# Kernel optimization log

Measured on AMD Instinct MI355X. Metric: run time of the kernel, lower is better.

The kernel has to match this reference:

```python
import jax, jax.numpy as jnp
import numpy as np

B, C = 16384, 5000
EPS = 1e-6
NEG_BIG = -1e30  # stand-in for -inf so rows with no positives stay finite


def setup_inputs() -> dict:
    key = jax.random.key(0)
    k1, k2, k3 = jax.random.split(key, 3)
    inp = jax.random.normal(k1, (B, C), dtype=jnp.float32)
    target = jax.random.randint(k2, (B, C), 0, 2, dtype=jnp.int32)
    weights = jax.random.uniform(k3, (B,), dtype=jnp.float32)
    return {"input": inp, "target": target, "weights": weights}


def reference(input, target, weights):
    # loss_ij = target_ij * log(clamp(sigmoid(x_ij), eps, 1-eps))
    logp = jnp.log(jnp.clip(jax.nn.sigmoid(input), EPS, 1.0 - EPS))  # [B, C], all < 0
    t = target.astype(logp.dtype)
    pos = t > 0
    # Original code: for rows with k positives, take max of loss over the positive
    # labels, then abs (entries are negative, so abs == negate). For k == 1 the
    # -sum over the row equals the same thing. Rows with zero positives stay 0.
    masked = jnp.where(pos, logp, NEG_BIG)            # [B, C]
    row_max = jnp.max(masked, axis=1)                 # [B]
    has_pos = jnp.any(pos, axis=1)                    # [B]
    loss1 = jnp.where(has_pos, -row_max, 0.0)         # [B], non-negative
    loss1 = loss1 * weights                           # instance-wise weights
    return jnp.mean(loss1)                            # aggregate='mean'
```

## Files before the change

kernel.cpp:

```cpp
#include <hip/hip_runtime.h>


#define NROWS 16384
#define NCOLS 5000
#define NVEC  (NCOLS / 4)
#define EPSF  1e-6f

typedef float fvec4 __attribute__((ext_vector_type(4)));
typedef int   ivec4 __attribute__((ext_vector_type(4)));

__global__ __launch_bounds__(256) void row_loss_kernel(
    const float* __restrict__ inp,
    const int*   __restrict__ tgt,
    const float* __restrict__ w,
    float*       __restrict__ row_loss)
{
    const int lane = threadIdx.x & 63;
    const int wid  = threadIdx.x >> 6;
    const int wave_global = blockIdx.x * 4 + wid;
    const float NEG = -3.0e38f;

    #pragma unroll
    for (int rr = 0; rr < 2; ++rr) {
        const int row = wave_global * 2 + rr;
        const fvec4* __restrict__ x4 = (const fvec4*)(inp + (size_t)row * NCOLS);
        const ivec4* __restrict__ t4 = (const ivec4*)(tgt + (size_t)row * NCOLS);

        float m = NEG;
        #pragma unroll
        for (int g = 0; g < 4; ++g) {
            fvec4 xv[5];
            ivec4 tv[5];
            #pragma unroll
            for (int k = 0; k < 5; ++k) {
                const int idx = (g * 5 + k) * 64 + lane;
                if (idx < NVEC) {
                    xv[k] = __builtin_nontemporal_load(x4 + idx);
                    tv[k] = __builtin_nontemporal_load(t4 + idx);
                } else {
                    xv[k] = (fvec4)0.0f;
                    tv[k] = (ivec4)0;
                }
            }
            #pragma unroll
            for (int k = 0; k < 5; ++k) {
                m = fmaxf(m, (tv[k][0] > 0) ? xv[k][0] : NEG);
                m = fmaxf(m, (tv[k][1] > 0) ? xv[k][1] : NEG);
                m = fmaxf(m, (tv[k][2] > 0) ? xv[k][2] : NEG);
                m = fmaxf(m, (tv[k][3] > 0) ? xv[k][3] : NEG);
            }
        }

        #pragma unroll
        for (int off = 32; off > 0; off >>= 1)
            m = fmaxf(m, __shfl_xor(m, off, 64));

        if (lane == 0) {
            float loss = 0.0f;
            if (m > -1.0e38f) {
                float p = 1.0f / (1.0f + __expf(-m));
                p = fminf(fmaxf(p, EPSF), 1.0f - EPSF);
                loss = -logf(p) * w[row];
            }
            row_loss[row] = loss;
        }
    }
}

__global__ __launch_bounds__(1024) void reduce_mean_kernel(
    const float* __restrict__ row_loss,
    float*       __restrict__ out)
{
    const fvec4* __restrict__ rl4 = (const fvec4*)row_loss;
    float s = 0.0f;
    #pragma unroll
    for (int j = 0; j < 4; ++j) {
        fvec4 v = rl4[threadIdx.x + j * 1024];
        s += (v[0] + v[1]) + (v[2] + v[3]);
    }

    #pragma unroll
    for (int off = 32; off > 0; off >>= 1)
        s += __shfl_xor(s, off, 64);

    __shared__ float ssum[16];
    const int lane = threadIdx.x & 63;
    const int wid  = threadIdx.x >> 6;
    if (lane == 0) ssum[wid] = s;
    __syncthreads();

    if (threadIdx.x == 0) {
        float tot = 0.0f;
        #pragma unroll
        for (int i = 0; i < 16; ++i) tot += ssum[i];
        out[0] = tot / (float)NROWS;
    }
}

extern "C" void kernel_launch(void* const* d_in, const int* in_sizes, int n_in,
                              void* d_out, int out_size, void* d_ws, size_t ws_size,
                              hipStream_t stream) {
    const float* inp = (const float*)d_in[0];
    const int*   tgt = (const int*)d_in[1];
    const float* w   = (const float*)d_in[2];
    float* row_loss  = (float*)d_ws;
    float* out       = (float*)d_out;

    row_loss_kernel<<<2048, 256, 0, stream>>>(inp, tgt, w, row_loss);
    reduce_mean_kernel<<<1, 1024, 0, stream>>>(row_loss, out);
}
```

Baseline: 565.7 us.

## Software-pipeline row loads with double buffers and one row per wave

Each wave now handles a single row, and the grid doubles to 4096 blocks. Loads are double-buffered so the next group of five vectors is in flight while the previous group is reduced. Four independent max accumulators shorten the dependency chain, and the per-load bounds checks are replaced by one tail-specific load. The aim is more memory-level parallelism and better latency hiding in a bandwidth-bound pass, at the cost of higher register pressure, which the launch-bounds occupancy hint tries to contain.

```diff
diff --git a/kernel.cpp b/kernel.cpp
--- a/kernel.cpp
+++ b/kernel.cpp
@@ -5,11 +5,58 @@
 #define NCOLS 5000
 #define NVEC  (NCOLS / 4)
 #define EPSF  1e-6f
+#define NEGF  -3.0e38f
 
 typedef float fvec4 __attribute__((ext_vector_type(4)));
 typedef int   ivec4 __attribute__((ext_vector_type(4)));
 
-__global__ __launch_bounds__(256) void row_loss_kernel(
+__device__ __forceinline__ void load5(const fvec4* __restrict__ x4,
+                                      const ivec4* __restrict__ t4,
+                                      int cbase, int lane,
+                                      fvec4 (&xv)[5], ivec4 (&tv)[5])
+{
+    #pragma unroll
+    for (int k = 0; k < 5; ++k) {
+        const int idx = (cbase + k) * 64 + lane;
+        xv[k] = __builtin_nontemporal_load(x4 + idx);
+        tv[k] = __builtin_nontemporal_load(t4 + idx);
+    }
+}
+
+__device__ __forceinline__ void load5_tail(const fvec4* __restrict__ x4,
+                                           const ivec4* __restrict__ t4,
+                                           int lane,
+                                           fvec4 (&xv)[5], ivec4 (&tv)[5])
+{
+    #pragma unroll
+    for (int k = 0; k < 4; ++k) {
+        const int idx = (15 + k) * 64 + lane;
+        xv[k] = __builtin_nontemporal_load(x4 + idx);
+        tv[k] = __builtin_nontemporal_load(t4 + idx);
+    }
+    const int idx = 19 * 64 + lane;
+    if (lane < 34) {
+        xv[4] = __builtin_nontemporal_load(x4 + idx);
+        tv[4] = __builtin_nontemporal_load(t4 + idx);
+    } else {
+        xv[4] = (fvec4)0.0f;
+        tv[4] = (ivec4)0;
+    }
+}
+
+__device__ __forceinline__ void consume5(const fvec4 (&xv)[5], const ivec4 (&tv)[5],
+                                         float& m0, float& m1, float& m2, float& m3)
+{
+    #pragma unroll
+    for (int k = 0; k < 5; ++k) {
+        m0 = fmaxf(m0, (tv[k][0] > 0) ? xv[k][0] : NEGF);
+        m1 = fmaxf(m1, (tv[k][1] > 0) ? xv[k][1] : NEGF);
+        m2 = fmaxf(m2, (tv[k][2] > 0) ? xv[k][2] : NEGF);
+        m3 = fmaxf(m3, (tv[k][3] > 0) ? xv[k][3] : NEGF);
+    }
+}
+
+__global__ __launch_bounds__(256, 4) void row_loss_kernel(
     const float* __restrict__ inp,
     const int*   __restrict__ tgt,
     const float* __restrict__ w,
@@ -17,53 +64,38 @@
 {
     const int lane = threadIdx.x & 63;
     const int wid  = threadIdx.x >> 6;
-    const int wave_global = blockIdx.x * 4 + wid;
-    const float NEG = -3.0e38f;
+    const int row  = blockIdx.x * 4 + wid;
+
+    const fvec4* __restrict__ x4 = (const fvec4*)(inp + (size_t)row * NCOLS);
+    const ivec4* __restrict__ t4 = (const ivec4*)(tgt + (size_t)row * NCOLS);
+
+    fvec4 xa[5], xb[5];
+    ivec4 ta[5], tb[5];
+    float m0 = NEGF, m1 = NEGF, m2 = NEGF, m3 = NEGF;
+
+    load5(x4, t4, 0, lane, xa, ta);
+    load5(x4, t4, 5, lane, xb, tb);
+    consume5(xa, ta, m0, m1, m2, m3);
+    load5(x4, t4, 10, lane, xa, ta);
+    consume5(xb, tb, m0, m1, m2, m3);
+    load5_tail(x4, t4, lane, xb, tb);
+    consume5(xa, ta, m0, m1, m2, m3);
+    consume5(xb, tb, m0, m1, m2, m3);
+
+    float m = fmaxf(fmaxf(m0, m1), fmaxf(m2, m3));
 
     #pragma unroll
-    for (int rr = 0; rr < 2; ++rr) {
-        const int row = wave_global * 2 + rr;
-        const fvec4* __restrict__ x4 = (const fvec4*)(inp + (size_t)row * NCOLS);
-        const ivec4* __restrict__ t4 = (const ivec4*)(tgt + (size_t)row * NCOLS);
+    for (int off = 32; off > 0; off >>= 1)
+        m = fmaxf(m, __shfl_xor(m, off, 64));
 
-        float m = NEG;
-        #pragma unroll
-        for (int g = 0; g < 4; ++g) {
-            fvec4 xv[5];
-            ivec4 tv[5];
-            #pragma unroll
-            for (int k = 0; k < 5; ++k) {
-                const int idx = (g * 5 + k) * 64 + lane;
-                if (idx < NVEC) {
-                    xv[k] = __builtin_nontemporal_load(x4 + idx);
-                    tv[k] = __builtin_nontemporal_load(t4 + idx);
-                } else {
-                    xv[k] = (fvec4)0.0f;
-                    tv[k] = (ivec4)0;
-                }
-            }
-            #pragma unroll
-            for (int k = 0; k < 5; ++k) {
-                m = fmaxf(m, (tv[k][0] > 0) ? xv[k][0] : NEG);
-                m = fmaxf(m, (tv[k][1] > 0) ? xv[k][1] : NEG);
-                m = fmaxf(m, (tv[k][2] > 0) ? xv[k][2] : NEG);
-                m = fmaxf(m, (tv[k][3] > 0) ? xv[k][3] : NEG);
-            }
+    if (lane == 0) {
+        float loss = 0.0f;
+        if (m > -1.0e38f) {
+            float p = 1.0f / (1.0f + __expf(-m));
+            p = fminf(fmaxf(p, EPSF), 1.0f - EPSF);
+            loss = -logf(p) * w[row];
         }
-
-        #pragma unroll
-        for (int off = 32; off > 0; off >>= 1)
-            m = fmaxf(m, __shfl_xor(m, off, 64));
-
-        if (lane == 0) {
-            float loss = 0.0f;
-            if (m > -1.0e38f) {
-                float p = 1.0f / (1.0f + __expf(-m));
-                p = fminf(fmaxf(p, EPSF), 1.0f - EPSF);
-                loss = -logf(p) * w[row];
-            }
-            row_loss[row] = loss;
-        }
+        row_loss[row] = loss;
     }
 }
 
@@ -106,6 +138,6 @@
     float* row_loss  = (float*)d_ws;
     float* out       = (float*)d_out;
 
-    row_loss_kernel<<<2048, 256, 0, stream>>>(inp, tgt, w, row_loss);
+    row_loss_kernel<<<4096, 256, 0, stream>>>(inp, tgt, w, row_loss);
     reduce_mean_kernel<<<1, 1024, 0, stream>>>(row_loss, out);
 }
```

After: 631.2 us. +11.6%, slower.

## Assign one row per wave with rolled loop and split max accumulators

Applied to the files above, without the earlier changes.

Each wave now handles a single row instead of two, so the grid doubles to 4096 blocks. The launch bound asks for 8 blocks per CU, and a rolled loop keeps register pressure low. The inner loop reads through byte-offset pointers, issuing all x loads before the target loads, and only the final partial chunk is bounds-checked. Four independent max accumulators shorten the dependency chain. The aim is more memory-level parallelism and occupancy on a bandwidth-bound streaming read; the cost is fewer loads in flight per wave.

```diff
diff --git a/kernel.cpp b/kernel.cpp
--- a/kernel.cpp
+++ b/kernel.cpp
@@ -5,11 +5,12 @@
 #define NCOLS 5000
 #define NVEC  (NCOLS / 4)
 #define EPSF  1e-6f
+#define NEGF  -3.0e38f
 
 typedef float fvec4 __attribute__((ext_vector_type(4)));
 typedef int   ivec4 __attribute__((ext_vector_type(4)));
 
-__global__ __launch_bounds__(256) void row_loss_kernel(
+__global__ __launch_bounds__(256, 8) void row_loss_kernel(
     const float* __restrict__ inp,
     const int*   __restrict__ tgt,
     const float* __restrict__ w,
@@ -17,53 +18,73 @@
 {
     const int lane = threadIdx.x & 63;
     const int wid  = threadIdx.x >> 6;
-    const int wave_global = blockIdx.x * 4 + wid;
-    const float NEG = -3.0e38f;
+    const int row  = blockIdx.x * 4 + wid;
+
+    const char* __restrict__ xb = (const char*)(inp + (size_t)row * NCOLS) + lane * 16;
+    const char* __restrict__ tb = (const char*)(tgt + (size_t)row * NCOLS) + lane * 16;
+
+    float m0 = NEGF, m1 = NEGF, m2 = NEGF, m3 = NEGF;
+
+    #pragma unroll 1
+    for (int g = 0; g < 4; ++g) {
+        fvec4 xv[4];
+        ivec4 tv[4];
+        #pragma unroll
+        for (int k = 0; k < 4; ++k)
+            xv[k] = __builtin_nontemporal_load((const fvec4*)(xb + k * 1024));
+        #pragma unroll
+        for (int k = 0; k < 4; ++k)
+            tv[k] = __builtin_nontemporal_load((const ivec4*)(tb + k * 1024));
+        #pragma unroll
+        for (int k = 0; k < 4; ++k) {
+            m0 = fmaxf(m0, (tv[k][0] > 0) ? xv[k][0] : NEGF);
+            m1 = fmaxf(m1, (tv[k][1] > 0) ? xv[k][1] : NEGF);
+            m2 = fmaxf(m2, (tv[k][2] > 0) ? xv[k][2] : NEGF);
+            m3 = fmaxf(m3, (tv[k][3] > 0) ? xv[k][3] : NEGF);
+        }
+        xb += 4096;
+        tb += 4096;
+    }
+
+    {
+        fvec4 xv[4];
+        ivec4 tv[4];
+        #pragma unroll
+        for (int k = 0; k < 3; ++k)
+            xv[k] = __builtin_nontemporal_load((const fvec4*)(xb + k * 1024));
+        #pragma unroll
+        for (int k = 0; k < 3; ++k)
+            tv[k] = __builtin_nontemporal_load((const ivec4*)(tb + k * 1024));
+        if (lane < 34) {
+            xv[3] = __builtin_nontemporal_load((const fvec4*)(xb + 3 * 1024));
+            tv[3] = __builtin_nontemporal_load((const ivec4*)(tb + 3 * 1024));
+        } else {
+            xv[3] = (fvec4)0.0f;
+            tv[3] = (ivec4)0;
+        }
+        #pragma unroll
+        for (int k = 0; k < 4; ++k) {
+            m0 = fmaxf(m0, (tv[k][0] > 0) ? xv[k][0] : NEGF);
+            m1 = fmaxf(m1, (tv[k][1] > 0) ? xv[k][1] : NEGF);
+            m2 = fmaxf(m2, (tv[k][2] > 0) ? xv[k][2] : NEGF);
+            m3 = fmaxf(m3, (tv[k][3] > 0) ? xv[k][3] : NEGF);
+        }
+    }
+
+    float m = fmaxf(fmaxf(m0, m1), fmaxf(m2, m3));
 
     #pragma unroll
-    for (int rr = 0; rr < 2; ++rr) {
-        const int row = wave_global * 2 + rr;
-        const fvec4* __restrict__ x4 = (const fvec4*)(inp + (size_t)row * NCOLS);
-        const ivec4* __restrict__ t4 = (const ivec4*)(tgt + (size_t)row * NCOLS);
+    for (int off = 32; off > 0; off >>= 1)
+        m = fmaxf(m, __shfl_xor(m, off, 64));
 
-        float m = NEG;
-        #pragma unroll
-        for (int g = 0; g < 4; ++g) {
-            fvec4 xv[5];
-            ivec4 tv[5];
-            #pragma unroll
-            for (int k = 0; k < 5; ++k) {
-                const int idx = (g * 5 + k) * 64 + lane;
-                if (idx < NVEC) {
-                    xv[k] = __builtin_nontemporal_load(x4 + idx);
-                    tv[k] = __builtin_nontemporal_load(t4 + idx);
-                } else {
-                    xv[k] = (fvec4)0.0f;
-                    tv[k] = (ivec4)0;
-                }
-            }
-            #pragma unroll
-            for (int k = 0; k < 5; ++k) {
-                m = fmaxf(m, (tv[k][0] > 0) ? xv[k][0] : NEG);
-                m = fmaxf(m, (tv[k][1] > 0) ? xv[k][1] : NEG);
-                m = fmaxf(m, (tv[k][2] > 0) ? xv[k][2] : NEG);
-                m = fmaxf(m, (tv[k][3] > 0) ? xv[k][3] : NEG);
-            }
+    if (lane == 0) {
+        float loss = 0.0f;
+        if (m > -1.0e38f) {
+            float p = 1.0f / (1.0f + __expf(-m));
+            p = fminf(fmaxf(p, EPSF), 1.0f - EPSF);
+            loss = -logf(p) * w[row];
         }
-
-        #pragma unroll
-        for (int off = 32; off > 0; off >>= 1)
-            m = fmaxf(m, __shfl_xor(m, off, 64));
-
-        if (lane == 0) {
-            float loss = 0.0f;
-            if (m > -1.0e38f) {
-                float p = 1.0f / (1.0f + __expf(-m));
-                p = fminf(fmaxf(p, EPSF), 1.0f - EPSF);
-                loss = -logf(p) * w[row];
-            }
-            row_loss[row] = loss;
-        }
+        row_loss[row] = loss;
     }
 }
 
@@ -106,6 +127,6 @@
     float* row_loss  = (float*)d_ws;
     float* out       = (float*)d_out;
 
-    row_loss_kernel<<<2048, 256, 0, stream>>>(inp, tgt, w, row_loss);
+    row_loss_kernel<<<4096, 256, 0, stream>>>(inp, tgt, w, row_loss);
     reduce_mean_kernel<<<1, 1024, 0, stream>>>(row_loss, out);
 }
```

Result: no change. 573.4 us (+1.4%).

## Stream each block's 8 rows as one contiguous span with block-wide row reduction

Applied to the files above, without the earlier changes.

Each 256-thread block now walks its 8 consecutive rows as one flat contiguous range of 10000 vec4s, so every load instruction is fully coalesced across the block and no lanes sit idle on partial row tails. Per-row maxima are kept in 8 registers, with row boundaries resolved at compile time, then reduced through wave shuffles and shared memory. Nontemporal loads are dropped and an occupancy hint is added to launch bounds. The trade-off is more registers, a shared-memory barrier, and less load batching per thread, since 39 sequential iterations replace the grouped five-load batches.

```diff
diff --git a/kernel.cpp b/kernel.cpp
--- a/kernel.cpp
+++ b/kernel.cpp
@@ -3,67 +3,90 @@
 
 #define NROWS 16384
 #define NCOLS 5000
-#define NVEC  (NCOLS / 4)
+#define NVEC_ROW 1250
+#define VEC_PER_BLOCK 10000
+#define ROWS_PER_BLOCK 8
+#define NBLOCKS 2048
 #define EPSF  1e-6f
+#define NEGF  -3.0e38f
 
 typedef float fvec4 __attribute__((ext_vector_type(4)));
 typedef int   ivec4 __attribute__((ext_vector_type(4)));
 
-__global__ __launch_bounds__(256) void row_loss_kernel(
+__global__ __launch_bounds__(256, 4) void row_loss_kernel(
     const float* __restrict__ inp,
     const int*   __restrict__ tgt,
     const float* __restrict__ w,
     float*       __restrict__ row_loss)
 {
-    const int lane = threadIdx.x & 63;
-    const int wid  = threadIdx.x >> 6;
-    const int wave_global = blockIdx.x * 4 + wid;
-    const float NEG = -3.0e38f;
+    const int tid  = threadIdx.x;
+    const int lane = tid & 63;
+    const int wid  = tid >> 6;
+
+    const size_t vbase = (size_t)blockIdx.x * VEC_PER_BLOCK;
+    const fvec4* __restrict__ x4 = (const fvec4*)inp + vbase;
+    const ivec4* __restrict__ t4 = (const ivec4*)tgt + vbase;
+
+    float m[ROWS_PER_BLOCK];
+    #pragma unroll
+    for (int r = 0; r < ROWS_PER_BLOCK; ++r) m[r] = NEGF;
 
     #pragma unroll
-    for (int rr = 0; rr < 2; ++rr) {
-        const int row = wave_global * 2 + rr;
-        const fvec4* __restrict__ x4 = (const fvec4*)(inp + (size_t)row * NCOLS);
-        const ivec4* __restrict__ t4 = (const ivec4*)(tgt + (size_t)row * NCOLS);
+    for (int j = 0; j < 39; ++j) {
+        const int l = j * 256 + tid;
+        const fvec4 xv = x4[l];
+        const ivec4 tv = t4[l];
+        const float mv = fmaxf(
+            fmaxf((tv[0] > 0) ? xv[0] : NEGF, (tv[1] > 0) ? xv[1] : NEGF),
+            fmaxf((tv[2] > 0) ? xv[2] : NEGF, (tv[3] > 0) ? xv[3] : NEGF));
+        const int c0 = (j * 256) / NVEC_ROW;
+        const int c1 = (j * 256 + 255) / NVEC_ROW;
+        if (c0 == c1) {
+            m[c0] = fmaxf(m[c0], mv);
+        } else {
+            const bool in0 = l < c1 * NVEC_ROW;
+            m[c0] = fmaxf(m[c0], in0 ? mv : NEGF);
+            m[c1] = fmaxf(m[c1], in0 ? NEGF : mv);
+        }
+    }
+    if (tid < 16) {
+        const int l = 39 * 256 + tid;
+        const fvec4 xv = x4[l];
+        const ivec4 tv = t4[l];
+        const float mv = fmaxf(
+            fmaxf((tv[0] > 0) ? xv[0] : NEGF, (tv[1] > 0) ? xv[1] : NEGF),
+            fmaxf((tv[2] > 0) ? xv[2] : NEGF, (tv[3] > 0) ? xv[3] : NEGF));
+        m[7] = fmaxf(m[7], mv);
+    }
 
-        float m = NEG;
-        #pragma unroll
-        for (int g = 0; g < 4; ++g) {
-            fvec4 xv[5];
-            ivec4 tv[5];
-            #pragma unroll
-            for (int k = 0; k < 5; ++k) {
-                const int idx = (g * 5 + k) * 64 + lane;
-                if (idx < NVEC) {
-                    xv[k] = __builtin_nontemporal_load(x4 + idx);
-                    tv[k] = __builtin_nontemporal_load(t4 + idx);
-                } else {
-                    xv[k] = (fvec4)0.0f;
-                    tv[k] = (ivec4)0;
-                }
-            }
-            #pragma unroll
-            for (int k = 0; k < 5; ++k) {
-                m = fmaxf(m, (tv[k][0] > 0) ? xv[k][0] : NEG);
-                m = fmaxf(m, (tv[k][1] > 0) ? xv[k][1] : NEG);
-                m = fmaxf(m, (tv[k][2] > 0) ? xv[k][2] : NEG);
-                m = fmaxf(m, (tv[k][3] > 0) ? xv[k][3] : NEG);
-            }
-        }
-
+    #pragma unroll
+    for (int r = 0; r < ROWS_PER_BLOCK; ++r) {
+        float v = m[r];
         #pragma unroll
         for (int off = 32; off > 0; off >>= 1)
-            m = fmaxf(m, __shfl_xor(m, off, 64));
+            v = fmaxf(v, __shfl_xor(v, off, 64));
+        m[r] = v;
+    }
 
-        if (lane == 0) {
-            float loss = 0.0f;
-            if (m > -1.0e38f) {
-                float p = 1.0f / (1.0f + __expf(-m));
-                p = fminf(fmaxf(p, EPSF), 1.0f - EPSF);
-                loss = -logf(p) * w[row];
-            }
-            row_loss[row] = loss;
+    __shared__ float sm[ROWS_PER_BLOCK][4];
+    if (lane == 0) {
+        #pragma unroll
+        for (int r = 0; r < ROWS_PER_BLOCK; ++r) sm[r][wid] = m[r];
+    }
+    __syncthreads();
+
+    if (tid < ROWS_PER_BLOCK) {
+        const int r = tid;
+        const float mx = fmaxf(fmaxf(sm[r][0], sm[r][1]),
+                               fmaxf(sm[r][2], sm[r][3]));
+        const int row = blockIdx.x * ROWS_PER_BLOCK + r;
+        float loss = 0.0f;
+        if (mx > -1.0e38f) {
+            float p = 1.0f / (1.0f + __expf(-mx));
+            p = fminf(fmaxf(p, EPSF), 1.0f - EPSF);
+            loss = -logf(p) * w[row];
         }
+        row_loss[row] = loss;
     }
 }
 
@@ -106,6 +129,6 @@
     float* row_loss  = (float*)d_ws;
     float* out       = (float*)d_out;
 
-    row_loss_kernel<<<2048, 256, 0, stream>>>(inp, tgt, w, row_loss);
+    row_loss_kernel<<<NBLOCKS, 256, 0, stream>>>(inp, tgt, w, row_loss);
     reduce_mean_kernel<<<1, 1024, 0, stream>>>(row_loss, out);
 }
```

Measured after the change: 610.9 us. 8.0% more time.
